# Kernel optimization log

Measured on AMD Instinct MI355X. Metric: run time of the kernel, lower is better.

Reference implementation:

```python
import jax, jax.numpy as jnp
import numpy as np

N_NODES = 100000
N_EDGES = 1600000
IN_CH = 256
OUT_CH = 64


def setup_inputs() -> dict:
    key = jax.random.key(0)
    k_x, k_e, k_w = jax.random.split(key, 3)
    x = jax.random.normal(k_x, (N_NODES, IN_CH), dtype=jnp.float32)
    edge_index = jax.random.randint(k_e, (2, N_EDGES), 0, N_NODES, dtype=jnp.int64)
    W = jax.random.normal(k_w, (IN_CH, OUT_CH), dtype=jnp.float32) / np.sqrt(IN_CH)
    b = jnp.zeros((OUT_CH,), dtype=jnp.float32)
    return {"x": x, "edge_index": edge_index, "W": W, "b": b}


def reference(x, edge_index, W, b):
    # GCNConv (PyG defaults: add self loops, symmetric deg^{-1/2} normalization,
    # linear transform + scatter-add aggregation, bias) followed by log_softmax.
    N = x.shape[0]
    loops = jnp.arange(N, dtype=edge_index.dtype)
    src = jnp.concatenate([edge_index[0], loops])  # message source (j)
    dst = jnp.concatenate([edge_index[1], loops])  # message target (i)

    # Degree (in-degree at dst with unit edge weights, incl. self loops)
    deg = jax.ops.segment_sum(jnp.ones_like(dst, dtype=x.dtype), dst, num_segments=N)
    dinv = jnp.where(deg > 0, jax.lax.rsqrt(deg), 0.0)
    norm = dinv[src] * dinv[dst]  # [E+N]

    h = x @ W  # [N, out] dense transform before gather (fewer channels to move)
    msg = h[src] * norm[:, None]  # gather + normalize
    agg = jax.ops.segment_sum(msg, dst, num_segments=N) + b  # scatter-add + bias
    return jax.nn.log_softmax(agg, axis=1)
```

## Files before the change

kernel.cpp:

```cpp
#include <hip/hip_runtime.h>
#include <math.h>

#define IN_CH 256
#define OUT_CH 64
#define BK_LOG 8
#define BK_NODES 256
#define NBK_CAP 1024
#define DIST_TILE 2048

typedef unsigned short ushort_t;
typedef unsigned int uint_t;
typedef __attribute__((ext_vector_type(8))) short bf16x8;
typedef __attribute__((ext_vector_type(4))) float f32x4;

__device__ __forceinline__ float b2f(uint_t u) {
    union { uint_t i; float f; } c; c.i = u << 16; return c.f;
}
__device__ __forceinline__ uint_t f2b(float f) {
    union { float f; uint_t i; } c; c.f = f;
    return (c.i + 0x7FFFu + ((c.i >> 16) & 1u)) >> 16;
}

__global__ void k_zero(int* __restrict__ p, int n) {
    int i = blockIdx.x * blockDim.x + threadIdx.x;
    if (i < n) p[i] = 0;
}

__global__ void k_bcount(const int* __restrict__ dst, int* __restrict__ bucketCnt,
                         int E, int nbk) {
    __shared__ int hist[NBK_CAP];
    const int tid = threadIdx.x;
    for (int b = tid; b < nbk; b += blockDim.x) hist[b] = 0;
    __syncthreads();
    int i = blockIdx.x * blockDim.x + tid;
    const int stride = gridDim.x * blockDim.x;
    for (; i < E; i += stride) atomicAdd(&hist[dst[i] >> BK_LOG], 1);
    __syncthreads();
    for (int b = tid; b < nbk; b += blockDim.x)
        if (hist[b]) atomicAdd(&bucketCnt[b], hist[b]);
}

__global__ void k_bscan(const int* __restrict__ bucketCnt, int* __restrict__ bucketOffs,
                        int* __restrict__ bucketCur, int nbk) {
    __shared__ int sdata[NBK_CAP];
    const int t = threadIdx.x;
    const int orig = (t < nbk) ? bucketCnt[t] : 0;
    sdata[t] = orig;
    __syncthreads();
    for (int off = 1; off < NBK_CAP; off <<= 1) {
        int v = (t >= off) ? sdata[t - off] : 0;
        __syncthreads();
        sdata[t] += v;
        __syncthreads();
    }
    if (t < nbk) {
        const int excl = sdata[t] - orig;
        bucketOffs[t] = excl;
        bucketCur[t] = excl;
        if (t == nbk - 1) bucketOffs[nbk] = sdata[t];
    }
}

__global__ __launch_bounds__(256) void k_distribute(
    const int* __restrict__ src, const int* __restrict__ dst,
    int* __restrict__ bucketCur, uint_t* __restrict__ packed,
    int E, int nbk)
{
    __shared__ int hist[NBK_CAP];
    __shared__ int base[NBK_CAP];
    const int tid = threadIdx.x;
    const int t0 = blockIdx.x * DIST_TILE;
    const int t1 = min(E, t0 + DIST_TILE);

    for (int b = tid; b < nbk; b += 256) hist[b] = 0;
    __syncthreads();
    for (int i = t0 + tid; i < t1; i += 256) atomicAdd(&hist[dst[i] >> BK_LOG], 1);
    __syncthreads();
    for (int b = tid; b < nbk; b += 256)
        base[b] = hist[b] ? atomicAdd(&bucketCur[b], hist[b]) : 0;
    __syncthreads();
    for (int i = t0 + tid; i < t1; i += 256) {
        const int d = dst[i];
        const int p = atomicAdd(&base[d >> BK_LOG], 1);
        packed[p] = (uint_t)src[i] | ((uint_t)(d & (BK_NODES - 1)) << 24);
    }
}

__global__ __launch_bounds__(256) void k_sortbucket(
    const uint_t* __restrict__ packed, const int* __restrict__ bucketOffs,
    int* __restrict__ offs, int* __restrict__ list, float* __restrict__ dinv, int N)
{
    __shared__ int hist[BK_NODES];
    __shared__ int scan[BK_NODES];
    const int tid = threadIdx.x;
    const int b = blockIdx.x;
    const int bo = bucketOffs[b], eo = bucketOffs[b + 1];

    hist[tid] = 0;
    __syncthreads();
    for (int i = bo + tid; i < eo; i += 256)
        atomicAdd(&hist[packed[i] >> 24], 1);
    __syncthreads();

    int v = hist[tid];
    scan[tid] = v;
    __syncthreads();
    for (int off = 1; off < BK_NODES; off <<= 1) {
        int u = (tid >= off) ? scan[tid - off] : 0;
        __syncthreads();
        scan[tid] += u;
        __syncthreads();
    }
    const int excl = scan[tid] - v;

    const int node = b * BK_NODES + tid;
    if (node < N) {
        offs[node] = bo + excl;
        dinv[node] = rsqrtf((float)v + 1.0f);
        if (node == N - 1) offs[N] = eo;
    }

    hist[tid] = bo + excl;
    __syncthreads();
    for (int i = bo + tid; i < eo; i += 256) {
        const uint_t pv = packed[i];
        const int p = atomicAdd(&hist[pv >> 24], 1);
        list[p] = (int)(pv & 0xFFFFFFu);
    }
}

__global__ __launch_bounds__(256) void k_prepW(const float* __restrict__ W,
                                               ushort_t* __restrict__ Wt) {
    const int j = blockIdx.x * 256 + threadIdx.x;
    const int col = j >> 8, k = j & 255;
    Wt[j] = (ushort_t)f2b(W[k * OUT_CH + col]);
}

__global__ __launch_bounds__(256) void k_gemm_mfma(
    const float* __restrict__ x, const ushort_t* __restrict__ Wt,
    const float* __restrict__ dinv, ushort_t* __restrict__ g2, int N)
{
    __shared__ ushort_t Ws[OUT_CH * IN_CH];
    const int tid = threadIdx.x;
    for (int i = tid * 8; i < OUT_CH * IN_CH; i += 256 * 8) {
        const int col = i >> 8;
        const uint_t byte = (uint_t)(i * 2) ^ ((uint_t)(col & 7) << 4);
        *(uint4*)((char*)Ws + byte) = *(const uint4*)&Wt[i];
    }
    __syncthreads();

    const int lane = tid & 63;
    const int l16 = lane & 15;
    const int lq = lane >> 4;
    const int rowbase = blockIdx.x * 64 + (tid >> 6) * 16;

    const int arow = min(rowbase + l16, N - 1);
    const float* __restrict__ xr = x + (size_t)arow * IN_CH + lq * 8;

    f32x4 acc[4];
#pragma unroll
    for (int c = 0; c < 4; ++c) acc[c] = (f32x4){0.f, 0.f, 0.f, 0.f};

    for (int k0 = 0; k0 < IN_CH; k0 += 32) {
        const float4 xa = *(const float4*)&xr[k0];
        const float4 xb = *(const float4*)&xr[k0 + 4];
        bf16x8 a;
        a[0] = (short)f2b(xa.x); a[1] = (short)f2b(xa.y);
        a[2] = (short)f2b(xa.z); a[3] = (short)f2b(xa.w);
        a[4] = (short)f2b(xb.x); a[5] = (short)f2b(xb.y);
        a[6] = (short)f2b(xb.z); a[7] = (short)f2b(xb.w);
        const int kk = (k0 + lq * 8) * 2;
#pragma unroll
        for (int c = 0; c < 4; ++c) {
            const int col = c * 16 + l16;
            const uint_t byte = (uint_t)(col * 512 + kk) ^ ((uint_t)(col & 7) << 4);
            const bf16x8 bfrag = *(const bf16x8*)((const char*)Ws + byte);
            acc[c] = __builtin_amdgcn_mfma_f32_16x16x32_bf16(a, bfrag, acc[c], 0, 0, 0);
        }
    }

#pragma unroll
    for (int r = 0; r < 4; ++r) {
        const int row = rowbase + lq * 4 + r;
        if (row < N) {
            const float dv = dinv[row];
            const size_t o = (size_t)row * OUT_CH;
            g2[o +  0 + l16] = (ushort_t)f2b(acc[0][r] * dv);
            g2[o + 16 + l16] = (ushort_t)f2b(acc[1][r] * dv);
            g2[o + 32 + l16] = (ushort_t)f2b(acc[2][r] * dv);
            g2[o + 48 + l16] = (ushort_t)f2b(acc[3][r] * dv);
        }
    }
}

__global__ void k_aggregate(const int* __restrict__ offs, const int* __restrict__ list,
                            const ushort_t* __restrict__ g2, const float* __restrict__ b,
                            float* __restrict__ out, int N)
{
    const int lane = threadIdx.x & 63;
    const int c2 = lane & 31;
    const int half = lane >> 5;
    int wid = (blockIdx.x * blockDim.x + threadIdx.x) >> 6;
    const int nw = (gridDim.x * blockDim.x) >> 6;
    const float bc0 = b[2 * c2], bc1 = b[2 * c2 + 1];

    for (int i = wid; i < N; i += nw) {
        const int start = offs[i];
        const int end = offs[i + 1];
        const int deg = end - start;
        float acc0 = 0.f, acc1 = 0.f;

        int e = start + half;
        for (; e + 6 < end; e += 8) {
            const int s0 = list[e];
            const int s1 = list[e + 2];
            const int s2 = list[e + 4];
            const int s3 = list[e + 6];
            const uint_t v0 = *(const uint_t*)&g2[(size_t)s0 * OUT_CH + c2 * 2];
            const uint_t v1 = *(const uint_t*)&g2[(size_t)s1 * OUT_CH + c2 * 2];
            const uint_t v2 = *(const uint_t*)&g2[(size_t)s2 * OUT_CH + c2 * 2];
            const uint_t v3 = *(const uint_t*)&g2[(size_t)s3 * OUT_CH + c2 * 2];
            acc0 += b2f(v0 & 0xFFFFu) + b2f(v1 & 0xFFFFu)
                  + b2f(v2 & 0xFFFFu) + b2f(v3 & 0xFFFFu);
            acc1 += b2f(v0 >> 16) + b2f(v1 >> 16)
                  + b2f(v2 >> 16) + b2f(v3 >> 16);
        }
        for (; e < end; e += 2) {
            const int s = list[e];
            const uint_t v = *(const uint_t*)&g2[(size_t)s * OUT_CH + c2 * 2];
            acc0 += b2f(v & 0xFFFFu);
            acc1 += b2f(v >> 16);
        }

        acc0 += __shfl_xor(acc0, 32);
        acc1 += __shfl_xor(acc1, 32);

        const uint_t sv = *(const uint_t*)&g2[(size_t)i * OUT_CH + c2 * 2];
        acc0 += b2f(sv & 0xFFFFu);
        acc1 += b2f(sv >> 16);

        const float dinv = rsqrtf((float)deg + 1.0f);
        const float z0 = acc0 * dinv + bc0;
        const float z1 = acc1 * dinv + bc1;

        float m = fmaxf(z0, z1);
#pragma unroll
        for (int off = 16; off; off >>= 1) m = fmaxf(m, __shfl_xor(m, off));
        float s = __expf(z0 - m) + __expf(z1 - m);
#pragma unroll
        for (int off = 16; off; off >>= 1) s += __shfl_xor(s, off);
        const float ls = __logf(s);

        if (half == 0) {
            *(float2*)&out[(size_t)i * OUT_CH + 2 * c2] =
                make_float2(z0 - m - ls, z1 - m - ls);
        }
    }
}

extern "C" void kernel_launch(void* const* d_in, const int* in_sizes, int n_in,
                              void* d_out, int out_size, void* d_ws, size_t ws_size,
                              hipStream_t stream) {
    const float* x  = (const float*)d_in[0];
    const int*   ei = (const int*)d_in[1];
    const float* W  = (const float*)d_in[2];
    const float* b  = (const float*)d_in[3];
    float* out = (float*)d_out;

    const int N = in_sizes[0] / IN_CH;
    const int E = in_sizes[1] / 2;
    const int* src = ei;
    const int* dst = ei + E;

    const int nbk = (N + BK_NODES - 1) >> BK_LOG;
    const int ndist = (E + DIST_TILE - 1) / DIST_TILE;

    char* p = (char*)d_ws;
    auto alloc = [&](size_t bytes) { char* q = p; p += (bytes + 255) & ~(size_t)255; return q; };
    int*      bucketCnt  = (int*)alloc(NBK_CAP * 4);
    int*      bucketOffs = (int*)alloc((NBK_CAP + 1) * 4);
    int*      bucketCur  = (int*)alloc(NBK_CAP * 4);
    ushort_t* Wt         = (ushort_t*)alloc((size_t)OUT_CH * IN_CH * 2);
    uint_t*   packed     = (uint_t*)alloc((size_t)E * 4);
    int*      list       = (int*)alloc((size_t)E * 4);
    int*      offs       = (int*)alloc((size_t)(N + 1) * 4);
    float*    dinv       = (float*)alloc((size_t)N * 4);
    ushort_t* g2         = (ushort_t*)alloc((size_t)N * OUT_CH * 2);

    k_zero      <<<(nbk + 255) / 256, 256, 0, stream>>>(bucketCnt, nbk);
    k_prepW     <<<(OUT_CH * IN_CH) / 256, 256, 0, stream>>>(W, Wt);
    k_bcount    <<<392, 256, 0, stream>>>(dst, bucketCnt, E, nbk);
    k_bscan     <<<1, NBK_CAP, 0, stream>>>(bucketCnt, bucketOffs, bucketCur, nbk);
    k_distribute<<<ndist, 256, 0, stream>>>(src, dst, bucketCur, packed, E, nbk);
    k_sortbucket<<<nbk, 256, 0, stream>>>(packed, bucketOffs, offs, list, dinv, N);
    k_gemm_mfma <<<(N + 63) / 64, 256, 0, stream>>>(x, Wt, dinv, g2, N);
    k_aggregate <<<4096, 256, 0, stream>>>(offs, list, g2, b, out, N);
}
```

Measured before the change: 151.5 us.

## Halve bucket size, deepen aggregate unroll, grow bcount grid, memset bucket counts

Bucket size drops from 256 to 128 nodes, giving about twice as many buckets (782 < NBK_CAP) so the sort kernel gets more, smaller blocks; only the first 128 threads take part in the histogram and scan. The aggregate inner loop is unrolled to 8 gathers per half-wave to keep more loads in flight. k_bcount's grid grows from 392 to 1024 blocks, and the zero kernel is replaced by hipMemsetAsync. The risks are more atomic traffic on bucket counters and idle threads in the sort kernel.

```diff
diff --git a/kernel.cpp b/kernel.cpp
--- a/kernel.cpp
+++ b/kernel.cpp
@@ -3,8 +3,8 @@
 
 #define IN_CH 256
 #define OUT_CH 64
-#define BK_LOG 8
-#define BK_NODES 256
+#define BK_LOG 7
+#define BK_NODES 128
 #define NBK_CAP 1024
 #define DIST_TILE 2048
 
@@ -19,11 +19,6 @@
 __device__ __forceinline__ uint_t f2b(float f) {
     union { float f; uint_t i; } c; c.f = f;
     return (c.i + 0x7FFFu + ((c.i >> 16) & 1u)) >> 16;
-}
-
-__global__ void k_zero(int* __restrict__ p, int n) {
-    int i = blockIdx.x * blockDim.x + threadIdx.x;
-    if (i < n) p[i] = 0;
 }
 
 __global__ void k_bcount(const int* __restrict__ dst, int* __restrict__ bucketCnt,
@@ -96,31 +91,31 @@
     const int b = blockIdx.x;
     const int bo = bucketOffs[b], eo = bucketOffs[b + 1];
 
-    hist[tid] = 0;
+    if (tid < BK_NODES) hist[tid] = 0;
     __syncthreads();
     for (int i = bo + tid; i < eo; i += 256)
         atomicAdd(&hist[packed[i] >> 24], 1);
     __syncthreads();
 
-    int v = hist[tid];
-    scan[tid] = v;
+    const int v = (tid < BK_NODES) ? hist[tid] : 0;
+    if (tid < BK_NODES) scan[tid] = v;
     __syncthreads();
     for (int off = 1; off < BK_NODES; off <<= 1) {
-        int u = (tid >= off) ? scan[tid - off] : 0;
-        __syncthreads();
-        scan[tid] += u;
-        __syncthreads();
-    }
-    const int excl = scan[tid] - v;
+        const int u = (tid >= off && tid < BK_NODES) ? scan[tid - off] : 0;
+        __syncthreads();
+        if (tid < BK_NODES) scan[tid] += u;
+        __syncthreads();
+    }
+    const int excl = (tid < BK_NODES) ? (scan[tid] - v) : 0;
 
     const int node = b * BK_NODES + tid;
-    if (node < N) {
+    if (tid < BK_NODES && node < N) {
         offs[node] = bo + excl;
         dinv[node] = rsqrtf((float)v + 1.0f);
         if (node == N - 1) offs[N] = eo;
     }
 
-    hist[tid] = bo + excl;
+    if (tid < BK_NODES) hist[tid] = bo + excl;
     __syncthreads();
     for (int i = bo + tid; i < eo; i += 256) {
         const uint_t pv = packed[i];
@@ -211,19 +206,19 @@
         float acc0 = 0.f, acc1 = 0.f;
 
         int e = start + half;
-        for (; e + 6 < end; e += 8) {
-            const int s0 = list[e];
-            const int s1 = list[e + 2];
-            const int s2 = list[e + 4];
-            const int s3 = list[e + 6];
-            const uint_t v0 = *(const uint_t*)&g2[(size_t)s0 * OUT_CH + c2 * 2];
-            const uint_t v1 = *(const uint_t*)&g2[(size_t)s1 * OUT_CH + c2 * 2];
-            const uint_t v2 = *(const uint_t*)&g2[(size_t)s2 * OUT_CH + c2 * 2];
-            const uint_t v3 = *(const uint_t*)&g2[(size_t)s3 * OUT_CH + c2 * 2];
-            acc0 += b2f(v0 & 0xFFFFu) + b2f(v1 & 0xFFFFu)
-                  + b2f(v2 & 0xFFFFu) + b2f(v3 & 0xFFFFu);
-            acc1 += b2f(v0 >> 16) + b2f(v1 >> 16)
-                  + b2f(v2 >> 16) + b2f(v3 >> 16);
+        for (; e + 14 < end; e += 16) {
+            int s[8];
+#pragma unroll
+            for (int j = 0; j < 8; ++j) s[j] = list[e + 2 * j];
+            uint_t v[8];
+#pragma unroll
+            for (int j = 0; j < 8; ++j)
+                v[j] = *(const uint_t*)&g2[(size_t)s[j] * OUT_CH + c2 * 2];
+#pragma unroll
+            for (int j = 0; j < 8; ++j) {
+                acc0 += b2f(v[j] & 0xFFFFu);
+                acc1 += b2f(v[j] >> 16);
+            }
         }
         for (; e < end; e += 2) {
             const int s = list[e];
@@ -287,9 +282,9 @@
     float*    dinv       = (float*)alloc((size_t)N * 4);
     ushort_t* g2         = (ushort_t*)alloc((size_t)N * OUT_CH * 2);
 
-    k_zero      <<<(nbk + 255) / 256, 256, 0, stream>>>(bucketCnt, nbk);
+    hipMemsetAsync(bucketCnt, 0, (size_t)nbk * 4, stream);
     k_prepW     <<<(OUT_CH * IN_CH) / 256, 256, 0, stream>>>(W, Wt);
-    k_bcount    <<<392, 256, 0, stream>>>(dst, bucketCnt, E, nbk);
+    k_bcount    <<<1024, 256, 0, stream>>>(dst, bucketCnt, E, nbk);
     k_bscan     <<<1, NBK_CAP, 0, stream>>>(bucketCnt, bucketOffs, bucketCur, nbk);
     k_distribute<<<ndist, 256, 0, stream>>>(src, dst, bucketCur, packed, E, nbk);
     k_sortbucket<<<nbk, 256, 0, stream>>>(packed, bucketOffs, offs, list, dinv, N);
```

Result: slower. 178.9 us (+18.1%).
